# Optimization experiments

Measured on AMD Instinct MI355X. Metric: run time of the kernel, lower is better.

The kernel has to match this reference:

```python
import jax, jax.numpy as jnp
import numpy as np

BIT = 8        # mantissa bits (incl. sign) for BFP activations
MAX_EXP = 7    # exponent bits for the shared block exponent
BLOCK = 32     # channels per BFP block
BN_EPS = 1e-5


def bfp_quantize(x, bit=BIT, max_exp=MAX_EXP, block=BLOCK):
    """Block-floating-point quantization along the channel axis.

    Channels are grouped into blocks of `block`; each block (per batch
    element and spatial position) shares one exponent = floor(log2(max|x|)),
    clamped to the `max_exp`-bit signed exponent range. Mantissas are
    rounded to `bit` bits (signed). Straight-through estimator for grads.
    """
    B, C, H, W = x.shape
    nb = C // block
    xb = x.reshape(B, nb, block, H, W)
    maxabs = jnp.max(jnp.abs(xb), axis=2, keepdims=True)          # [B,nb,1,H,W]
    e = jnp.floor(jnp.log2(jnp.maximum(maxabs, 1e-12)))
    e = jnp.clip(e, -(2.0 ** (max_exp - 1)), 2.0 ** (max_exp - 1) - 1.0)
    step = jnp.exp2(e) * (2.0 ** -(bit - 1))                       # quantization step
    qmax = 2.0 ** (bit - 1) - 1.0
    q = jnp.clip(jnp.round(xb / step), -(qmax + 1.0), qmax) * step
    q = q.reshape(B, C, H, W)
    # straight-through estimator (as used for quantization-aware training)
    return x + jax.lax.stop_gradient(q - x)


def setup_inputs() -> dict:
    key = jax.random.key(0)
    k1, k2, k3, k4 = jax.random.split(key, 4)
    x = jax.random.normal(k1, (32, 256, 56, 56), jnp.float32)
    W = jax.random.normal(k2, (256, 256, 3, 3), jnp.float32) * 0.05  # OIHW
    gamma = jax.random.uniform(k3, (256,), jnp.float32, 0.5, 1.5)
    beta = jax.random.normal(k4, (256,), jnp.float32) * 0.1
    return {"x": x, "W": W, "gamma": gamma, "beta": beta}


def reference(x, W, gamma, beta):
    # 1) block-floating-point quantize activations
    xq = bfp_quantize(x)
    # 2) 3x3 conv, stride 1, pad 1 (DSConv2d forward math)
    y = jax.lax.conv_general_dilated(
        xq, W, window_strides=(1, 1), padding=((1, 1), (1, 1)),
        dimension_numbers=("NCHW", "OIHW", "NCHW"))
    # 3) BatchNorm2d (training-mode batch statistics, biased variance)
    mean = jnp.mean(y, axis=(0, 2, 3))
    var = jnp.var(y, axis=(0, 2, 3))
    inv = jax.lax.rsqrt(var + BN_EPS)
    yn = (y - mean[None, :, None, None]) * inv[None, :, None, None]
    yn = yn * gamma[None, :, None, None] + beta[None, :, None, None]
    # 4) ReLU
    return jax.nn.relu(yn)
```

## Files before the change

kernel.cpp:

```cpp
#include <hip/hip_runtime.h>
#include <hip/hip_bf16.h>
#include <cstdint>
#include <cstddef>

#define BATCH 32
#define CIN   256
#define COUT  256
#define HH    56
#define WW    56
#define HP    60
#define WPAD  64
#define KTOT  2304
#define MTOT  100352
#define HW    3136
#define NBLK  392

typedef __attribute__((ext_vector_type(4))) float  f32x4;
typedef __attribute__((ext_vector_type(8))) short  short8;
typedef __attribute__((ext_vector_type(4))) short  short4v;

__global__ void zeropad_kernel(unsigned short* __restrict__ xq)
{
    const int b   = blockIdx.y;
    const int idx = blockIdx.x * 256 + threadIdx.x;
    const int pos = idx >> 5;
    const int ch  = (idx & 31) * 8;
    int hp, wp;
    if (pos < 256) {
        int r = pos >> 6;
        hp = (r == 0) ? 0 : 56 + r;
        wp = pos & 63;
    } else {
        int i2 = pos - 256;
        int c  = i2 & 7;
        hp = (i2 >> 3) + 1;
        wp = (c == 0) ? 0 : 56 + c;
    }
    short8 z = {0, 0, 0, 0, 0, 0, 0, 0};
    *reinterpret_cast<short8*>(xq + (((size_t)b * HP + hp) * WPAD + wp) * CIN + ch) = z;
}

__global__ void quant_kernel(const float* __restrict__ x, unsigned short* __restrict__ xq)
{
    const int hb  = blockIdx.x;
    const int b   = blockIdx.y;
    const int tid = threadIdx.x;
    const int hh  = tid >> 6;
    const int w   = tid & 63;
    const int h   = hb * 4 + hh;
    if (w >= WW) return;
    for (int cb = 0; cb < 8; ++cb) {
        float v[32];
        float mx = 0.f;
        const float* xp = x + (((size_t)b * CIN + cb * 32) * HH + h) * WW + w;
#pragma unroll
        for (int c = 0; c < 32; ++c) {
            float t = xp[(size_t)c * HH * WW];
            v[c] = t;
            mx = fmaxf(mx, fabsf(t));
        }
        float m = fmaxf(mx, 1e-12f);
        int e;
        frexpf(m, &e);
        e -= 1;
        e = (e < -64) ? -64 : ((e > 63) ? 63 : e);
        float step = exp2f((float)(e - 7));
        float inv  = exp2f((float)(7 - e));
        unsigned short qb[32];
#pragma unroll
        for (int c = 0; c < 32; ++c) {
            float q = rintf(v[c] * inv);
            q = fminf(fmaxf(q, -128.f), 127.f);
            float val = q * step;
            __hip_bfloat16 bv = __float2bfloat16(val);
            qb[c] = *reinterpret_cast<unsigned short*>(&bv);
        }
        unsigned short* dst = xq + (((size_t)b * HP + (h + 1)) * WPAD + (w + 1)) * CIN + cb * 32;
#pragma unroll
        for (int i = 0; i < 4; ++i)
            *reinterpret_cast<short8*>(dst + i * 8) = *reinterpret_cast<const short8*>(qb + i * 8);
    }
}

__global__ void wrepack_kernel(const float* __restrict__ Wsrc, unsigned short* __restrict__ WrP)
{
    int E = blockIdx.x * 256 + threadIdx.x;
    if (E >= 36 * 16384) return;
    int kt = E >> 14;
    int r  = E & 16383;
    int tg = r >> 10;
    int kk = (r >> 9) & 1;
    int l  = (r >> 3) & 63;
    int i  = E & 7;
    int n  = tg * 16 + (l & 15);
    int c  = (kt & 3) * 64 + kk * 32 + (l >> 4) * 8 + i;
    int j  = kt >> 2;
    float val = Wsrc[((size_t)n * CIN + c) * 9 + j];
    __hip_bfloat16 bv = __float2bfloat16(val);
    WrP[E] = *reinterpret_cast<unsigned short*>(&bv);
}

__device__ __forceinline__ void gload_lds16(const void* g, void* l)
{
    __builtin_amdgcn_global_load_lds((const __attribute__((address_space(1))) void*)g,
                                     (__attribute__((address_space(3))) void*)l, 16, 0, 0);
}
#define VMWAIT(n) do { asm volatile("s_waitcnt vmcnt(" #n ")" ::: "memory"); } while (0)
#define PRIO(n)   __builtin_amdgcn_s_setprio(n)
#define SBAR()    __builtin_amdgcn_s_barrier()

#define MFMA_PH(p)                                                                        \
    _Pragma("unroll")                                                                     \
    for (int kk = 0; kk < 2; ++kk)                                                        \
        _Pragma("unroll")                                                                 \
        for (int jj = 0; jj < 2; ++jj)                                                    \
            _Pragma("unroll")                                                             \
            for (int ni = 0; ni < 4; ++ni)                                                \
                acc[2 * (p) + jj][ni] = __builtin_amdgcn_mfma_f32_16x16x32_bf16(          \
                    afv[jj][kk], bfv[ni][kk], acc[2 * (p) + jj][ni], 0, 0, 0);

#define LDA_PH(p)                                                                         \
    _Pragma("unroll")                                                                     \
    for (int jj = 0; jj < 2; ++jj)                                                        \
        _Pragma("unroll")                                                                 \
        for (int kk = 0; kk < 2; ++kk)                                                    \
            afv[jj][kk] = *(const short8*)(Ac + (wm * 8 + 2 * (p) + jj) * 1024 +          \
                                           kk * 512 + lane * 8);

#define KT(ktE, A3, B2, SB, SA, A3n, B2n, VMT) do {                                       \
    const int kt_ = (ktE);                                                                \
    const unsigned short* Ac = lds + (A3) * 16384;                                        \
    const unsigned short* Bc = lds + 49152 + (B2) * 16384;                                \
    short8 bfv[4][2], afv[2][2];                                                          \
                                                                   \
    _Pragma("unroll")                                                                     \
    for (int ni = 0; ni < 4; ++ni)                                                        \
        _Pragma("unroll")                                                                 \
        for (int kk = 0; kk < 2; ++kk)                                                    \
            bfv[ni][kk] = *(const short8*)(Bc + (wn * 4 + ni) * 1024 + kk * 512 +         \
                                           lane * 8);                                     \
    LDA_PH(0);                                                                            \
    if (SB) stgB(kt_ + 1, 0, (B2n));                                                      \
    SBAR(); PRIO(1); MFMA_PH(0); PRIO(0); SBAR();                                         \
                                                                   \
    LDA_PH(1);                                                                            \
    if (SB) stgB(kt_ + 1, 1, (B2n));                                                      \
    SBAR(); PRIO(1); MFMA_PH(1); PRIO(0); SBAR();                                         \
                                                                   \
    LDA_PH(2);                                                                            \
    if (SA) stgA(kt_ + 2, 0, (A3n));                                                      \
    SBAR(); PRIO(1); MFMA_PH(2); PRIO(0); SBAR();                                         \
                                                                   \
    LDA_PH(3);                                                                            \
    if (SA) stgA(kt_ + 2, 1, (A3n));                                                      \
    SBAR(); PRIO(1); MFMA_PH(3); PRIO(0);                                                 \
    VMT;                                                                                  \
    SBAR();                                                                               \
} while (0)

template <int Y16>
__global__ __launch_bounds__(512) void conv_gemm_kernel(const unsigned short* __restrict__ xq,
                                                        const unsigned short* __restrict__ WrP,
                                                        float* __restrict__ out,
                                                        unsigned short* __restrict__ y16,
                                                        float* __restrict__ sums)
{
    extern __shared__ __align__(16) unsigned short lds[];

    const int bid  = blockIdx.x;
    const int blk  = (bid & 7) * 49 + (bid >> 3);
    const int m0   = blk * 256;
    const int tid  = threadIdx.x;
    const int wv   = tid >> 6;
    const int lane = tid & 63;
    const int ln   = lane & 15;
    const int kg   = lane >> 4;
    const int wm   = wv >> 2;
    const int wn   = wv & 3;

    int abase2[2];
#pragma unroll
    for (int hh = 0; hh < 2; ++hh) {
        int row = m0 + (hh * 8 + wv) * 16 + ln;
        int bb  = row / HW;
        int hw  = row - bb * HW;
        int h   = hw / WW;
        int w   = hw - h * WW;
        abase2[hh] = ((bb * HP + h) * WPAD + w) * CIN + kg * 8;
    }

    auto stgA = [&](int kt2, int h, int a3) {
        const int j  = kt2 >> 2;
        const int kh = j / 3, kw = j - 3 * kh;
        const int aoff = (kh * WPAD + kw) * CIN + (kt2 & 3) * 64;
        unsigned short* dst = lds + a3 * 16384 + (h * 8 + wv) * 1024;
#pragma unroll
        for (int q = 0; q < 2; ++q)
            gload_lds16(xq + abase2[h] + aoff + q * 32, (void*)(dst + q * 512));
    };
    auto stgB = [&](int kt1, int h, int b2) {
        const unsigned short* src = WrP + kt1 * 16384 + (h * 8 + wv) * 1024 + lane * 8;
        unsigned short* dst = lds + 49152 + b2 * 16384 + (h * 8 + wv) * 1024;
#pragma unroll
        for (int q = 0; q < 2; ++q)
            gload_lds16(src + q * 512, (void*)(dst + q * 512));
    };

    f32x4 acc[8][4];
#pragma unroll
    for (int i = 0; i < 8; ++i)
#pragma unroll
        for (int jn = 0; jn < 4; ++jn) acc[i][jn] = (f32x4){0.f, 0.f, 0.f, 0.f};

    stgA(0, 0, 0); stgA(0, 1, 0);
    stgA(1, 0, 1); stgA(1, 1, 1);
    stgB(0, 0, 0); stgB(0, 1, 0);
    VMWAIT(0);
    SBAR();

    for (int it = 0; it < 5; ++it) {
        const int k0 = it * 6;
        KT(k0 + 0, 0, 0, 1, 1, 2, 1, VMWAIT(4));
        KT(k0 + 1, 1, 1, 1, 1, 0, 0, VMWAIT(4));
        KT(k0 + 2, 2, 0, 1, 1, 1, 1, VMWAIT(4));
        KT(k0 + 3, 0, 1, 1, 1, 2, 0, VMWAIT(4));
        KT(k0 + 4, 1, 0, 1, 1, 0, 1, VMWAIT(4));
        KT(k0 + 5, 2, 1, 1, 1, 1, 0, VMWAIT(4));
    }
    KT(30, 0, 0, 1, 1, 2, 1, VMWAIT(4));
    KT(31, 1, 1, 1, 1, 0, 0, VMWAIT(4));
    KT(32, 2, 0, 1, 1, 1, 1, VMWAIT(4));
    KT(33, 0, 1, 1, 1, 2, 0, VMWAIT(4));
    KT(34, 1, 0, 1, 0, 0, 1, VMWAIT(0));
    KT(35, 2, 1, 0, 0, 0, 0, (void)0);

#pragma unroll
    for (int jn = 0; jn < 4; ++jn) {
        const int n = wn * 64 + jn * 16 + ln;
        float s = 0.f, s2 = 0.f;
#pragma unroll
        for (int i = 0; i < 8; ++i) {
            const int row = m0 + wm * 128 + i * 16 + kg * 4;
            const int bb  = row / HW;
            const int hw  = row - bb * HW;
            f32x4 v = acc[i][jn];
            s  += v[0] + v[1] + v[2] + v[3];
            s2 += v[0] * v[0] + v[1] * v[1] + v[2] * v[2] + v[3] * v[3];
            const size_t idx = (size_t)bb * (COUT * HW) + (size_t)n * HW + hw;
            if (Y16) {
                short4v hv;
#pragma unroll
                for (int r = 0; r < 4; ++r) {
                    __hip_bfloat16 bv = __float2bfloat16(v[r]);
                    hv[r] = *reinterpret_cast<short*>(&bv);
                }
                *reinterpret_cast<short4v*>(&y16[idx]) = hv;
            } else {
                *reinterpret_cast<f32x4*>(&out[idx]) = v;
            }
        }
        s  += __shfl_xor(s, 16);  s  += __shfl_xor(s, 32);
        s2 += __shfl_xor(s2, 16); s2 += __shfl_xor(s2, 32);
        if (kg == 0) {
            atomicAdd(&sums[n], s);
            atomicAdd(&sums[COUT + n], s2);
        }
    }
}

__global__ void bn_apply32_kernel(float* __restrict__ y, const float* __restrict__ sums,
                                  const float* __restrict__ gamma, const float* __restrict__ beta)
{
    const int o = blockIdx.x, b = blockIdx.y;
    const float N = (float)(BATCH * HH * WW);
    const float mean = sums[o] / N;
    const float var  = sums[COUT + o] / N - mean * mean;
    const float inv  = 1.f / sqrtf(var + 1e-5f);
    const float a  = gamma[o] * inv;
    const float bb = beta[o] - mean * a;
    float* p = y + ((size_t)b * COUT + o) * HW;
    for (int i = threadIdx.x; i < 784; i += 256) {
        f32x4 v = *reinterpret_cast<const f32x4*>(p + i * 4);
#pragma unroll
        for (int r = 0; r < 4; ++r) v[r] = fmaxf(v[r] * a + bb, 0.f);
        *reinterpret_cast<f32x4*>(p + i * 4) = v;
    }
}

__global__ void bn_apply16_kernel(const unsigned short* __restrict__ y16, float* __restrict__ out,
                                  const float* __restrict__ sums,
                                  const float* __restrict__ gamma, const float* __restrict__ beta)
{
    const int o = blockIdx.x, b = blockIdx.y;
    const float N = (float)(BATCH * HH * WW);
    const float mean = sums[o] / N;
    const float var  = sums[COUT + o] / N - mean * mean;
    const float inv  = 1.f / sqrtf(var + 1e-5f);
    const float a  = gamma[o] * inv;
    const float bb = beta[o] - mean * a;
    const unsigned short* p16 = y16 + ((size_t)b * COUT + o) * HW;
    float* p = out + ((size_t)b * COUT + o) * HW;
    for (int i = threadIdx.x; i < 784; i += 256) {
        short4v hv = *reinterpret_cast<const short4v*>(p16 + i * 4);
        f32x4 v;
#pragma unroll
        for (int r = 0; r < 4; ++r) {
            unsigned int bits = ((unsigned int)(unsigned short)hv[r]) << 16;
            float f = *reinterpret_cast<float*>(&bits);
            v[r] = fmaxf(f * a + bb, 0.f);
        }
        *reinterpret_cast<f32x4*>(p + i * 4) = v;
    }
}

extern "C" void kernel_launch(void* const* d_in, const int* in_sizes, int n_in,
                              void* d_out, int out_size, void* d_ws, size_t ws_size,
                              hipStream_t stream)
{
    const float* x     = (const float*)d_in[0];
    const float* Wsrc  = (const float*)d_in[1];
    const float* gamma = (const float*)d_in[2];
    const float* beta  = (const float*)d_in[3];
    float* out = (float*)d_out;

    char* ws = (char*)d_ws;
    const size_t XQ_BYTES  = (size_t)BATCH * HP * WPAD * CIN * 2;
    const size_t WR_BYTES  = (size_t)36 * 16384 * 2;
    const size_t SUM_BYTES = 4096;
    const size_t Y16_BYTES = (size_t)BATCH * COUT * HW * 2;
    unsigned short* xq = (unsigned short*)ws;
    unsigned short* wr = (unsigned short*)(ws + XQ_BYTES);
    float* sums = (float*)(ws + XQ_BYTES + WR_BYTES);
    unsigned short* y16 = (unsigned short*)(ws + XQ_BYTES + WR_BYTES + SUM_BYTES);
    const bool useY16 = ws_size >= XQ_BYTES + WR_BYTES + SUM_BYTES + Y16_BYTES;

    hipMemsetAsync(sums, 0, 2 * COUT * sizeof(float), stream);

    zeropad_kernel<<<dim3(88, BATCH), 256, 0, stream>>>(xq);
    quant_kernel<<<dim3(14, BATCH), 256, 0, stream>>>(x, xq);
    wrepack_kernel<<<2304, 256, 0, stream>>>(Wsrc, wr);

    if (useY16) {
        hipFuncSetAttribute(reinterpret_cast<const void*>(&conv_gemm_kernel<1>),
                            hipFuncAttributeMaxDynamicSharedMemorySize, 163840);
        conv_gemm_kernel<1><<<NBLK, 512, 163840, stream>>>(xq, wr, out, y16, sums);
        bn_apply16_kernel<<<dim3(COUT, BATCH), 256, 0, stream>>>(y16, out, sums, gamma, beta);
    } else {
        hipFuncSetAttribute(reinterpret_cast<const void*>(&conv_gemm_kernel<0>),
                            hipFuncAttributeMaxDynamicSharedMemorySize, 163840);
        conv_gemm_kernel<0><<<NBLK, 512, 163840, stream>>>(xq, wr, out, y16, sums);
        bn_apply32_kernel<<<dim3(COUT, BATCH), 256, 0, stream>>>(out, sums, gamma, beta);
    }
}
```

Baseline: 220.5 us.

## Shrink conv GEMM M-tile to 224 for 448 blocks, fuse prep kernels, nontemporal stores

Cuts the conv GEMM M tile from 256 to 224 rows, giving 448 workgroups instead of 392. The aim is a better fit across the 256 CUs: the old grid left many CUs idle in the second wave. Only 7 of 8 waves now stage A tiles, so the vmcnt waits are split per wave and the LDS footprint shrinks. The zero-pad and weight-repack kernels are merged into one launch, and the output and intermediate stores and loads use nontemporal hints. In exchange, each block reuses its B tile across fewer rows and one wave sits idle during A staging.

```diff
diff --git a/kernel.cpp b/kernel.cpp
--- a/kernel.cpp
+++ b/kernel.cpp
@@ -13,31 +13,52 @@
 #define KTOT  2304
 #define MTOT  100352
 #define HW    3136
-#define NBLK  392
+#define MT    224
+#define NBLK  448
 
 typedef __attribute__((ext_vector_type(4))) float  f32x4;
 typedef __attribute__((ext_vector_type(8))) short  short8;
 typedef __attribute__((ext_vector_type(4))) short  short4v;
 
-__global__ void zeropad_kernel(unsigned short* __restrict__ xq)
-{
-    const int b   = blockIdx.y;
-    const int idx = blockIdx.x * 256 + threadIdx.x;
-    const int pos = idx >> 5;
-    const int ch  = (idx & 31) * 8;
-    int hp, wp;
-    if (pos < 256) {
-        int r = pos >> 6;
-        hp = (r == 0) ? 0 : 56 + r;
-        wp = pos & 63;
+__global__ void prep_kernel(const float* __restrict__ Wsrc, unsigned short* __restrict__ WrP,
+                            unsigned short* __restrict__ xq)
+{
+    const int bid = blockIdx.x;
+    const int tid = threadIdx.x;
+    if (bid < 2304) {
+        int E  = bid * 256 + tid;
+        int kt = E >> 14;
+        int r  = E & 16383;
+        int tg = r >> 10;
+        int kk = (r >> 9) & 1;
+        int l  = (r >> 3) & 63;
+        int i  = E & 7;
+        int n  = tg * 16 + (l & 15);
+        int c  = (kt & 3) * 64 + kk * 32 + (l >> 4) * 8 + i;
+        int j  = kt >> 2;
+        float val = Wsrc[((size_t)n * CIN + c) * 9 + j];
+        __hip_bfloat16 bv = __float2bfloat16(val);
+        WrP[E] = *reinterpret_cast<unsigned short*>(&bv);
     } else {
-        int i2 = pos - 256;
-        int c  = i2 & 7;
-        hp = (i2 >> 3) + 1;
-        wp = (c == 0) ? 0 : 56 + c;
-    }
-    short8 z = {0, 0, 0, 0, 0, 0, 0, 0};
-    *reinterpret_cast<short8*>(xq + (((size_t)b * HP + hp) * WPAD + wp) * CIN + ch) = z;
+        const int zbid = bid - 2304;
+        const int b    = zbid / 88;
+        const int idx  = (zbid % 88) * 256 + tid;
+        const int pos  = idx >> 5;
+        const int ch   = (idx & 31) * 8;
+        int hp, wp;
+        if (pos < 256) {
+            int r = pos >> 6;
+            hp = (r == 0) ? 0 : 56 + r;
+            wp = pos & 63;
+        } else {
+            int i2 = pos - 256;
+            int c  = i2 & 7;
+            hp = (i2 >> 3) + 1;
+            wp = (c == 0) ? 0 : 56 + c;
+        }
+        short8 z = {0, 0, 0, 0, 0, 0, 0, 0};
+        *reinterpret_cast<short8*>(xq + (((size_t)b * HP + hp) * WPAD + wp) * CIN + ch) = z;
+    }
 }
 
 __global__ void quant_kernel(const float* __restrict__ x, unsigned short* __restrict__ xq)
@@ -82,55 +103,38 @@
     }
 }
 
-__global__ void wrepack_kernel(const float* __restrict__ Wsrc, unsigned short* __restrict__ WrP)
-{
-    int E = blockIdx.x * 256 + threadIdx.x;
-    if (E >= 36 * 16384) return;
-    int kt = E >> 14;
-    int r  = E & 16383;
-    int tg = r >> 10;
-    int kk = (r >> 9) & 1;
-    int l  = (r >> 3) & 63;
-    int i  = E & 7;
-    int n  = tg * 16 + (l & 15);
-    int c  = (kt & 3) * 64 + kk * 32 + (l >> 4) * 8 + i;
-    int j  = kt >> 2;
-    float val = Wsrc[((size_t)n * CIN + c) * 9 + j];
-    __hip_bfloat16 bv = __float2bfloat16(val);
-    WrP[E] = *reinterpret_cast<unsigned short*>(&bv);
-}
-
 __device__ __forceinline__ void gload_lds16(const void* g, void* l)
 {
     __builtin_amdgcn_global_load_lds((const __attribute__((address_space(1))) void*)g,
                                      (__attribute__((address_space(3))) void*)l, 16, 0, 0);
 }
 #define VMWAIT(n) do { asm volatile("s_waitcnt vmcnt(" #n ")" ::: "memory"); } while (0)
+#define VMSTEADY  do { if (wv < 7) VMWAIT(4); else VMWAIT(0); } while (0)
 #define PRIO(n)   __builtin_amdgcn_s_setprio(n)
 #define SBAR()    __builtin_amdgcn_s_barrier()
 
-#define MFMA_PH(p)                                                                        \
+#define LDA2(f0)                                                                          \
+    _Pragma("unroll")                                                                     \
+    for (int jj = 0; jj < 2; ++jj)                                                        \
+        _Pragma("unroll")                                                                 \
+        for (int kk = 0; kk < 2; ++kk)                                                    \
+            afv[jj][kk] = *(const short8*)(Ac + (wm * 7 + (f0) + jj) * 1024 +             \
+                                           kk * 512 + lane * 8);
+
+#define MFMA_2F(f0)                                                                       \
     _Pragma("unroll")                                                                     \
     for (int kk = 0; kk < 2; ++kk)                                                        \
         _Pragma("unroll")                                                                 \
         for (int jj = 0; jj < 2; ++jj)                                                    \
             _Pragma("unroll")                                                             \
             for (int ni = 0; ni < 4; ++ni)                                                \
-                acc[2 * (p) + jj][ni] = __builtin_amdgcn_mfma_f32_16x16x32_bf16(          \
-                    afv[jj][kk], bfv[ni][kk], acc[2 * (p) + jj][ni], 0, 0, 0);
-
-#define LDA_PH(p)                                                                         \
-    _Pragma("unroll")                                                                     \
-    for (int jj = 0; jj < 2; ++jj)                                                        \
-        _Pragma("unroll")                                                                 \
-        for (int kk = 0; kk < 2; ++kk)                                                    \
-            afv[jj][kk] = *(const short8*)(Ac + (wm * 8 + 2 * (p) + jj) * 1024 +          \
-                                           kk * 512 + lane * 8);
+                acc[(f0) + jj][ni] = __builtin_amdgcn_mfma_f32_16x16x32_bf16(             \
+                    afv[jj][kk], bfv[ni][kk], acc[(f0) + jj][ni], 0, 0, 0);
 
 #define KT(ktE, A3, B2, SB, SA, A3n, B2n, VMT) do {                                       \
     const int kt_ = (ktE);                                                                \
-    const unsigned short* Ac = lds + (A3) * 16384;                                        \
-    const unsigned short* Bc = lds + 49152 + (B2) * 16384;                                \
+    const unsigned short* Ac = lds + (A3) * 14336;                                        \
+    const unsigned short* Bc = lds + 43008 + (B2) * 16384;                                \
     short8 bfv[4][2], afv[2][2];                                                          \
                                                                    \
     _Pragma("unroll")                                                                     \
@@ -139,21 +143,30 @@
         for (int kk = 0; kk < 2; ++kk)                                                    \
             bfv[ni][kk] = *(const short8*)(Bc + (wn * 4 + ni) * 1024 + kk * 512 +         \
                                            lane * 8);                                     \
-    LDA_PH(0);                                                                            \
+    LDA2(0);                                                                              \
     if (SB) stgB(kt_ + 1, 0, (B2n));                                                      \
-    SBAR(); PRIO(1); MFMA_PH(0); PRIO(0); SBAR();                                         \
+    SBAR(); PRIO(1); MFMA_2F(0); PRIO(0); SBAR();                                         \
                                                                    \
-    LDA_PH(1);                                                                            \
+    LDA2(2);                                                                              \
     if (SB) stgB(kt_ + 1, 1, (B2n));                                                      \
-    SBAR(); PRIO(1); MFMA_PH(1); PRIO(0); SBAR();                                         \
+    SBAR(); PRIO(1); MFMA_2F(2); PRIO(0); SBAR();                                         \
                                                                    \
-    LDA_PH(2);                                                                            \
+    LDA2(4);                                                                              \
     if (SA) stgA(kt_ + 2, 0, (A3n));                                                      \
-    SBAR(); PRIO(1); MFMA_PH(2); PRIO(0); SBAR();                                         \
-                                                                   \
-    LDA_PH(3);                                                                            \
+    SBAR(); PRIO(1); MFMA_2F(4); PRIO(0); SBAR();                                         \
+                                                          \
+    _Pragma("unroll")                                                                     \
+    for (int kk = 0; kk < 2; ++kk)                                                        \
+        afv[0][kk] = *(const short8*)(Ac + (wm * 7 + 6) * 1024 + kk * 512 + lane * 8);    \
     if (SA) stgA(kt_ + 2, 1, (A3n));                                                      \
-    SBAR(); PRIO(1); MFMA_PH(3); PRIO(0);                                                 \
+    SBAR(); PRIO(1);                                                                      \
+    _Pragma("unroll")                                                                     \
+    for (int kk = 0; kk < 2; ++kk)                                                        \
+        _Pragma("unroll")                                                                 \
+        for (int ni = 0; ni < 4; ++ni)                                                    \
+            acc[6][ni] = __builtin_amdgcn_mfma_f32_16x16x32_bf16(                         \
+                afv[0][kk], bfv[ni][kk], acc[6][ni], 0, 0, 0);                            \
+    PRIO(0);                                                                              \
     VMT;                                                                                  \
     SBAR();                                                                               \
 } while (0)
@@ -168,8 +181,8 @@
     extern __shared__ __align__(16) unsigned short lds[];
 
     const int bid  = blockIdx.x;
-    const int blk  = (bid & 7) * 49 + (bid >> 3);
-    const int m0   = blk * 256;
+    const int blk  = (bid & 7) * 56 + (bid >> 3);
+    const int m0   = blk * MT;
     const int tid  = threadIdx.x;
     const int wv   = tid >> 6;
     const int lane = tid & 63;
@@ -180,35 +193,37 @@
 
     int abase2[2];
 #pragma unroll
-    for (int hh = 0; hh < 2; ++hh) {
-        int row = m0 + (hh * 8 + wv) * 16 + ln;
+    for (int q = 0; q < 2; ++q) {
+        int g   = q * 7 + ((wv < 7) ? wv : 0);
+        int row = m0 + g * 16 + ln;
         int bb  = row / HW;
         int hw  = row - bb * HW;
         int h   = hw / WW;
         int w   = hw - h * WW;
-        abase2[hh] = ((bb * HP + h) * WPAD + w) * CIN + kg * 8;
+        abase2[q] = ((bb * HP + h) * WPAD + w) * CIN + kg * 8;
     }
 
     auto stgA = [&](int kt2, int h, int a3) {
+        if (wv >= 7) return;
         const int j  = kt2 >> 2;
         const int kh = j / 3, kw = j - 3 * kh;
         const int aoff = (kh * WPAD + kw) * CIN + (kt2 & 3) * 64;
-        unsigned short* dst = lds + a3 * 16384 + (h * 8 + wv) * 1024;
-#pragma unroll
-        for (int q = 0; q < 2; ++q)
-            gload_lds16(xq + abase2[h] + aoff + q * 32, (void*)(dst + q * 512));
+        unsigned short* dst = lds + a3 * 14336 + (7 * h + wv) * 1024;
+#pragma unroll
+        for (int kk = 0; kk < 2; ++kk)
+            gload_lds16(xq + abase2[h] + aoff + kk * 32, (void*)(dst + kk * 512));
     };
     auto stgB = [&](int kt1, int h, int b2) {
         const unsigned short* src = WrP + kt1 * 16384 + (h * 8 + wv) * 1024 + lane * 8;
-        unsigned short* dst = lds + 49152 + b2 * 16384 + (h * 8 + wv) * 1024;
+        unsigned short* dst = lds + 43008 + b2 * 16384 + (h * 8 + wv) * 1024;
 #pragma unroll
         for (int q = 0; q < 2; ++q)
             gload_lds16(src + q * 512, (void*)(dst + q * 512));
     };
 
-    f32x4 acc[8][4];
-#pragma unroll
-    for (int i = 0; i < 8; ++i)
+    f32x4 acc[7][4];
+#pragma unroll
+    for (int i = 0; i < 7; ++i)
 #pragma unroll
         for (int jn = 0; jn < 4; ++jn) acc[i][jn] = (f32x4){0.f, 0.f, 0.f, 0.f};
 
@@ -220,17 +235,17 @@
 
     for (int it = 0; it < 5; ++it) {
         const int k0 = it * 6;
-        KT(k0 + 0, 0, 0, 1, 1, 2, 1, VMWAIT(4));
-        KT(k0 + 1, 1, 1, 1, 1, 0, 0, VMWAIT(4));
-        KT(k0 + 2, 2, 0, 1, 1, 1, 1, VMWAIT(4));
-        KT(k0 + 3, 0, 1, 1, 1, 2, 0, VMWAIT(4));
-        KT(k0 + 4, 1, 0, 1, 1, 0, 1, VMWAIT(4));
-        KT(k0 + 5, 2, 1, 1, 1, 1, 0, VMWAIT(4));
-    }
-    KT(30, 0, 0, 1, 1, 2, 1, VMWAIT(4));
-    KT(31, 1, 1, 1, 1, 0, 0, VMWAIT(4));
-    KT(32, 2, 0, 1, 1, 1, 1, VMWAIT(4));
-    KT(33, 0, 1, 1, 1, 2, 0, VMWAIT(4));
+        KT(k0 + 0, 0, 0, 1, 1, 2, 1, VMSTEADY);
+        KT(k0 + 1, 1, 1, 1, 1, 0, 0, VMSTEADY);
+        KT(k0 + 2, 2, 0, 1, 1, 1, 1, VMSTEADY);
+        KT(k0 + 3, 0, 1, 1, 1, 2, 0, VMSTEADY);
+        KT(k0 + 4, 1, 0, 1, 1, 0, 1, VMSTEADY);
+        KT(k0 + 5, 2, 1, 1, 1, 1, 0, VMSTEADY);
+    }
+    KT(30, 0, 0, 1, 1, 2, 1, VMSTEADY);
+    KT(31, 1, 1, 1, 1, 0, 0, VMSTEADY);
+    KT(32, 2, 0, 1, 1, 1, 1, VMSTEADY);
+    KT(33, 0, 1, 1, 1, 2, 0, VMSTEADY);
     KT(34, 1, 0, 1, 0, 0, 1, VMWAIT(0));
     KT(35, 2, 1, 0, 0, 0, 0, (void)0);
 
@@ -239,8 +254,8 @@
         const int n = wn * 64 + jn * 16 + ln;
         float s = 0.f, s2 = 0.f;
 #pragma unroll
-        for (int i = 0; i < 8; ++i) {
-            const int row = m0 + wm * 128 + i * 16 + kg * 4;
+        for (int i = 0; i < 7; ++i) {
+            const int row = m0 + wm * 112 + i * 16 + kg * 4;
             const int bb  = row / HW;
             const int hw  = row - bb * HW;
             f32x4 v = acc[i][jn];
@@ -254,9 +269,9 @@
                     __hip_bfloat16 bv = __float2bfloat16(v[r]);
                     hv[r] = *reinterpret_cast<short*>(&bv);
                 }
-                *reinterpret_cast<short4v*>(&y16[idx]) = hv;
+                __builtin_nontemporal_store(hv, reinterpret_cast<short4v*>(&y16[idx]));
             } else {
-                *reinterpret_cast<f32x4*>(&out[idx]) = v;
+                __builtin_nontemporal_store(v, reinterpret_cast<f32x4*>(&out[idx]));
             }
         }
         s  += __shfl_xor(s, 16);  s  += __shfl_xor(s, 32);
@@ -301,7 +316,8 @@
     const unsigned short* p16 = y16 + ((size_t)b * COUT + o) * HW;
     float* p = out + ((size_t)b * COUT + o) * HW;
     for (int i = threadIdx.x; i < 784; i += 256) {
-        short4v hv = *reinterpret_cast<const short4v*>(p16 + i * 4);
+        short4v hv = __builtin_nontemporal_load(
+            reinterpret_cast<const short4v*>(p16 + i * 4));
         f32x4 v;
 #pragma unroll
         for (int r = 0; r < 4; ++r) {
@@ -309,7 +325,7 @@
             float f = *reinterpret_cast<float*>(&bits);
             v[r] = fmaxf(f * a + bb, 0.f);
         }
-        *reinterpret_cast<f32x4*>(p + i * 4) = v;
+        __builtin_nontemporal_store(v, reinterpret_cast<f32x4*>(p + i * 4));
     }
 }
 
@@ -336,19 +352,18 @@
 
     hipMemsetAsync(sums, 0, 2 * COUT * sizeof(float), stream);
 
-    zeropad_kernel<<<dim3(88, BATCH), 256, 0, stream>>>(xq);
+    prep_kernel<<<5120, 256, 0, stream>>>(Wsrc, wr, xq);
     quant_kernel<<<dim3(14, BATCH), 256, 0, stream>>>(x, xq);
-    wrepack_kernel<<<2304, 256, 0, stream>>>(Wsrc, wr);
 
     if (useY16) {
         hipFuncSetAttribute(reinterpret_cast<const void*>(&conv_gemm_kernel<1>),
-                            hipFuncAttributeMaxDynamicSharedMemorySize, 163840);
-        conv_gemm_kernel<1><<<NBLK, 512, 163840, stream>>>(xq, wr, out, y16, sums);
+                            hipFuncAttributeMaxDynamicSharedMemorySize, 151552);
+        conv_gemm_kernel<1><<<NBLK, 512, 151552, stream>>>(xq, wr, out, y16, sums);
         bn_apply16_kernel<<<dim3(COUT, BATCH), 256, 0, stream>>>(y16, out, sums, gamma, beta);
     } else {
         hipFuncSetAttribute(reinterpret_cast<const void*>(&conv_gemm_kernel<0>),
-                            hipFuncAttributeMaxDynamicSharedMemorySize, 163840);
-        conv_gemm_kernel<0><<<NBLK, 512, 163840, stream>>>(xq, wr, out, y16, sums);
+                            hipFuncAttributeMaxDynamicSharedMemorySize, 151552);
+        conv_gemm_kernel<0><<<NBLK, 512, 151552, stream>>>(xq, wr, out, y16, sums);
         bn_apply32_kernel<<<dim3(COUT, BATCH), 256, 0, stream>>>(out, sums, gamma, beta);
     }
 }
```

After: 210.9 us. -4.4%, faster.
